# Optimization experiments

Measured on AMD Instinct MI355X. Metric: run time of the kernel, lower is better.

The kernel has to match this reference:

```python
import jax, jax.numpy as jnp
import numpy as np

IN_F = 1024
OUT_F = 4096
BATCH = 1024

def setup_inputs() -> dict:
    key = jax.random.key(0)
    k1, k2, k3, k4 = jax.random.split(key, 4)
    s = np.sqrt(IN_F).astype(np.float32)  # weight init range, as in reset_parameters
    x = jax.random.normal(k1, (BATCH, IN_F), dtype=jnp.float32)
    weights = jax.random.uniform(k2, (OUT_F, IN_F), minval=-s, maxval=s, dtype=jnp.float32)
    centers = 0.1 * jax.random.normal(k3, (OUT_F, IN_F), dtype=jnp.float32)
    # sigmas ~ U(in-0.5, in+0.5); inv_covar = 1/sigmas
    sigmas = jax.random.uniform(k4, (OUT_F, IN_F), minval=IN_F - 0.5, maxval=IN_F + 0.5, dtype=jnp.float32)
    inv_covar = 1.0 / sigmas
    return {"x": x, "weights": weights, "centers": centers, "inv_covar": inv_covar}

def reference(x, weights, centers, inv_covar):
    # linear part with FGN bias: b_i = -sum_j W_ij * C_ij
    biases = -jnp.sum(weights * centers, axis=-1)  # (O,)
    l = x @ weights.T + biases                      # (B, O)
    # diag Mahalanobis: g_bi = sum_j (x_bj - c_ij)^2 * ic_ij^2
    # expanded to GEMMs to avoid the (B, O, I) broadcast intermediate
    ic2 = inv_covar * inv_covar                     # (O, I)
    g = ((x * x) @ ic2.T
         - 2.0 * (x @ (centers * ic2).T)
         + jnp.sum(centers * centers * ic2, axis=-1))  # (B, O)
    return l * jnp.exp(-g)
```

## Files before the change

kernel.cpp:

```cpp
#include <hip/hip_runtime.h>
#include <hip/hip_bf16.h>
#include <stdint.h>


typedef __attribute__((ext_vector_type(8))) __bf16 bf16x8;
typedef __attribute__((ext_vector_type(4))) float f32x4;

__device__ __forceinline__ unsigned short f2bf(float f) {
  union { float f; unsigned int u; } v; v.f = f;
  unsigned int u = v.u;
  unsigned int r = (u + 0x7FFFu + ((u >> 16) & 1u)) >> 16;
  return (unsigned short)r;
}

__global__ __launch_bounds__(256) void prep_rows(
    const float* __restrict__ W, const float* __restrict__ C,
    const float* __restrict__ IC,
    unsigned short* __restrict__ Wb, unsigned short* __restrict__ I2b,
    unsigned short* __restrict__ M2b,
    float* __restrict__ bias, float* __restrict__ dvec) {
  const int wave = threadIdx.x >> 6;
  const int lane = threadIdx.x & 63;
  const int row  = blockIdx.x * 4 + wave;
  const float4* W4 = (const float4*)W + (size_t)row * 256;
  const float4* C4 = (const float4*)C + (size_t)row * 256;
  const float4* I4 = (const float4*)IC + (size_t)row * 256;
  ushort4* Wo = (ushort4*)Wb + (size_t)row * 256;
  ushort4* Io = (ushort4*)I2b + (size_t)row * 256;
  ushort4* Mo = (ushort4*)M2b + (size_t)row * 256;
  float swc = 0.f, sd = 0.f;
#pragma unroll
  for (int p = 0; p < 4; ++p) {
    int idx = lane + p * 64;
    float4 w = W4[idx], c = C4[idx], ic = I4[idx];
    float i2x = ic.x * ic.x, i2y = ic.y * ic.y, i2z = ic.z * ic.z, i2w = ic.w * ic.w;
    swc += w.x * c.x + w.y * c.y + w.z * c.z + w.w * c.w;
    sd  += c.x * c.x * i2x + c.y * c.y * i2y + c.z * c.z * i2z + c.w * c.w * i2w;
    ushort4 a, b, m;
    a.x = f2bf(w.x); a.y = f2bf(w.y); a.z = f2bf(w.z); a.w = f2bf(w.w);
    b.x = f2bf(i2x); b.y = f2bf(i2y); b.z = f2bf(i2z); b.w = f2bf(i2w);
    m.x = f2bf(-2.f * c.x * i2x); m.y = f2bf(-2.f * c.y * i2y);
    m.z = f2bf(-2.f * c.z * i2z); m.w = f2bf(-2.f * c.w * i2w);
    Wo[idx] = a; Io[idx] = b; Mo[idx] = m;
  }
#pragma unroll
  for (int off = 32; off > 0; off >>= 1) {
    swc += __shfl_down(swc, off);
    sd  += __shfl_down(sd, off);
  }
  if (lane == 0) { bias[row] = -swc; dvec[row] = sd; }
}

__global__ __launch_bounds__(256) void prep_x(
    const float* __restrict__ X,
    unsigned short* __restrict__ Xb, unsigned short* __restrict__ Qb) {
  int idx = blockIdx.x * 256 + threadIdx.x;
  float4 x = ((const float4*)X)[idx];
  ushort4 a, b;
  a.x = f2bf(x.x); a.y = f2bf(x.y); a.z = f2bf(x.z); a.w = f2bf(x.w);
  b.x = f2bf(x.x * x.x); b.y = f2bf(x.y * x.y);
  b.z = f2bf(x.z * x.z); b.w = f2bf(x.w * x.w);
  ((ushort4*)Xb)[idx] = a;
  ((ushort4*)Qb)[idx] = b;
}

#define GLD16(gp, lp)                                                          \
  __builtin_amdgcn_global_load_lds(                                            \
      (const __attribute__((address_space(1))) unsigned int*)(gp),             \
      (__attribute__((address_space(3))) unsigned int*)(lp), 16, 0, 0)

__global__ __launch_bounds__(256) void fgn_gemm(
    const unsigned short* __restrict__ Xb, const unsigned short* __restrict__ Qb,
    const unsigned short* __restrict__ Wb, const unsigned short* __restrict__ I2b,
    const unsigned short* __restrict__ M2b,
    const float* __restrict__ bias, const float* __restrict__ dvec,
    float* __restrict__ out) {
  __shared__ unsigned short sx[64 * 32];
  __shared__ unsigned short sq[64 * 32];
  __shared__ unsigned short sw[128 * 32];
  __shared__ unsigned short si[128 * 32];
  __shared__ unsigned short sm[128 * 32];
  const int t = threadIdx.x;
  const int m0 = blockIdx.y * 64;
  const int n0 = blockIdx.x * 128;

  const int arow = t >> 2;
  const int acol = (t & 3) * 8;
  const unsigned short* gx  = Xb  + (size_t)(m0 + arow) * 1024 + acol;
  const unsigned short* gq  = Qb  + (size_t)(m0 + arow) * 1024 + acol;
  const unsigned short* gw0 = Wb  + (size_t)(n0 + arow) * 1024 + acol;
  const unsigned short* gw1 = Wb  + (size_t)(n0 + 64 + arow) * 1024 + acol;
  const unsigned short* gi0 = I2b + (size_t)(n0 + arow) * 1024 + acol;
  const unsigned short* gi1 = I2b + (size_t)(n0 + 64 + arow) * 1024 + acol;
  const unsigned short* gm0 = M2b + (size_t)(n0 + arow) * 1024 + acol;
  const unsigned short* gm1 = M2b + (size_t)(n0 + 64 + arow) * 1024 + acol;

  const int wave = t >> 6, lane = t & 63;
  const int wm = (wave & 1) * 32;
  const int wn = (wave >> 1) * 64;
  const int fm = lane & 15;
  const int q  = lane >> 4;

  f32x4 accL[2][4], accG[2][4];
#pragma unroll
  for (int mt = 0; mt < 2; ++mt)
#pragma unroll
    for (int nt = 0; nt < 4; ++nt) { accL[mt][nt] = (f32x4)0.f; accG[mt][nt] = (f32x4)0.f; }

  for (int k0 = 0; k0 < 1024; k0 += 32) {
    __syncthreads();
    GLD16(gx,  &sx[t * 8]);
    GLD16(gq,  &sq[t * 8]);
    GLD16(gw0, &sw[t * 8]);
    GLD16(gw1, &sw[2048 + t * 8]);
    GLD16(gi0, &si[t * 8]);
    GLD16(gi1, &si[2048 + t * 8]);
    GLD16(gm0, &sm[t * 8]);
    GLD16(gm1, &sm[2048 + t * 8]);
    gx += 32; gq += 32; gw0 += 32; gw1 += 32;
    gi0 += 32; gi1 += 32; gm0 += 32; gm1 += 32;
    __syncthreads();

    bf16x8 ax[2], aq[2], bw[4], bi[4], bm[4];
#pragma unroll
    for (int mt = 0; mt < 2; ++mt) {
      int r = wm + mt * 16 + fm;
      ax[mt] = *(const bf16x8*)&sx[r * 32 + q * 8];
      aq[mt] = *(const bf16x8*)&sq[r * 32 + q * 8];
    }
#pragma unroll
    for (int nt = 0; nt < 4; ++nt) {
      int r = wn + nt * 16 + fm;
      bw[nt] = *(const bf16x8*)&sw[r * 32 + q * 8];
      bi[nt] = *(const bf16x8*)&si[r * 32 + q * 8];
      bm[nt] = *(const bf16x8*)&sm[r * 32 + q * 8];
    }
#pragma unroll
    for (int mt = 0; mt < 2; ++mt)
#pragma unroll
      for (int nt = 0; nt < 4; ++nt) {
        accL[mt][nt] = __builtin_amdgcn_mfma_f32_16x16x32_bf16(ax[mt], bw[nt], accL[mt][nt], 0, 0, 0);
        accG[mt][nt] = __builtin_amdgcn_mfma_f32_16x16x32_bf16(aq[mt], bi[nt], accG[mt][nt], 0, 0, 0);
        accG[mt][nt] = __builtin_amdgcn_mfma_f32_16x16x32_bf16(ax[mt], bm[nt], accG[mt][nt], 0, 0, 0);
      }
  }

#pragma unroll
  for (int nt = 0; nt < 4; ++nt) {
    int gcol = n0 + wn + nt * 16 + fm;
    float bn = bias[gcol], dn = dvec[gcol];
#pragma unroll
    for (int mt = 0; mt < 2; ++mt) {
      int growb = m0 + wm + mt * 16 + q * 4;
#pragma unroll
      for (int r = 0; r < 4; ++r) {
        float l = accL[mt][nt][r] + bn;
        float g = accG[mt][nt][r] + dn;
        out[(size_t)(growb + r) * 4096 + gcol] = l * __expf(-g);
      }
    }
  }
}

extern "C" void kernel_launch(void* const* d_in, const int* in_sizes, int n_in,
                              void* d_out, int out_size, void* d_ws, size_t ws_size,
                              hipStream_t stream) {
  const float* x  = (const float*)d_in[0];
  const float* W  = (const float*)d_in[1];
  const float* C  = (const float*)d_in[2];
  const float* IC = (const float*)d_in[3];
  float* out = (float*)d_out;

  char* ws = (char*)d_ws;
  unsigned short* Wb  = (unsigned short*)(ws);
  unsigned short* I2b = (unsigned short*)(ws + (8u << 20));
  unsigned short* M2b = (unsigned short*)(ws + (16u << 20));
  unsigned short* Xb  = (unsigned short*)(ws + (24u << 20));
  unsigned short* Qb  = (unsigned short*)(ws + (26u << 20));
  float* bias = (float*)(ws + (28u << 20));
  float* dvec = (float*)(ws + (28u << 20) + 16384);

  hipLaunchKernelGGL(prep_rows, dim3(1024), dim3(256), 0, stream, W, C, IC,
                     Wb, I2b, M2b, bias, dvec);
  hipLaunchKernelGGL(prep_x, dim3(1024), dim3(256), 0, stream, x, Xb, Qb);
  hipLaunchKernelGGL(fgn_gemm, dim3(32, 16), dim3(256), 0, stream,
                     Xb, Qb, Wb, I2b, M2b, bias, dvec, out);
}
```

Measured before the change: 139.1 us.

## Enlarge GEMM tile, double-buffer LDS, swizzle, use 32x32 MFMA, merge prep kernels

Merges the two prep kernels into one launch. The GEMM tile grows from 64x128 to 128x128, switches to 32x32x16 MFMA instructions, and double-buffers LDS so the next K-slice is loaded while the current one is computed. LDS columns are XOR-swizzled to cut bank conflicts. The larger tile halves the grid to 256 blocks at one block per CU, which lowers occupancy and may under-fill the 256 CUs while improving data reuse.

```diff
diff --git a/kernel.cpp b/kernel.cpp
--- a/kernel.cpp
+++ b/kernel.cpp
@@ -4,7 +4,7 @@
 
 
 typedef __attribute__((ext_vector_type(8))) __bf16 bf16x8;
-typedef __attribute__((ext_vector_type(4))) float f32x4;
+typedef __attribute__((ext_vector_type(16))) float f32x16;
 
 __device__ __forceinline__ unsigned short f2bf(float f) {
   union { float f; unsigned int u; } v; v.f = f;
@@ -13,55 +13,59 @@
   return (unsigned short)r;
 }
 
-__global__ __launch_bounds__(256) void prep_rows(
-    const float* __restrict__ W, const float* __restrict__ C,
-    const float* __restrict__ IC,
+__global__ __launch_bounds__(256) void prep(
+    const float* __restrict__ X, const float* __restrict__ W,
+    const float* __restrict__ C, const float* __restrict__ IC,
     unsigned short* __restrict__ Wb, unsigned short* __restrict__ I2b,
     unsigned short* __restrict__ M2b,
+    unsigned short* __restrict__ Xb, unsigned short* __restrict__ Qb,
     float* __restrict__ bias, float* __restrict__ dvec) {
-  const int wave = threadIdx.x >> 6;
-  const int lane = threadIdx.x & 63;
-  const int row  = blockIdx.x * 4 + wave;
-  const float4* W4 = (const float4*)W + (size_t)row * 256;
-  const float4* C4 = (const float4*)C + (size_t)row * 256;
-  const float4* I4 = (const float4*)IC + (size_t)row * 256;
-  ushort4* Wo = (ushort4*)Wb + (size_t)row * 256;
-  ushort4* Io = (ushort4*)I2b + (size_t)row * 256;
-  ushort4* Mo = (ushort4*)M2b + (size_t)row * 256;
-  float swc = 0.f, sd = 0.f;
-#pragma unroll
-  for (int p = 0; p < 4; ++p) {
-    int idx = lane + p * 64;
-    float4 w = W4[idx], c = C4[idx], ic = I4[idx];
-    float i2x = ic.x * ic.x, i2y = ic.y * ic.y, i2z = ic.z * ic.z, i2w = ic.w * ic.w;
-    swc += w.x * c.x + w.y * c.y + w.z * c.z + w.w * c.w;
-    sd  += c.x * c.x * i2x + c.y * c.y * i2y + c.z * c.z * i2z + c.w * c.w * i2w;
-    ushort4 a, b, m;
-    a.x = f2bf(w.x); a.y = f2bf(w.y); a.z = f2bf(w.z); a.w = f2bf(w.w);
-    b.x = f2bf(i2x); b.y = f2bf(i2y); b.z = f2bf(i2z); b.w = f2bf(i2w);
-    m.x = f2bf(-2.f * c.x * i2x); m.y = f2bf(-2.f * c.y * i2y);
-    m.z = f2bf(-2.f * c.z * i2z); m.w = f2bf(-2.f * c.w * i2w);
-    Wo[idx] = a; Io[idx] = b; Mo[idx] = m;
-  }
-#pragma unroll
-  for (int off = 32; off > 0; off >>= 1) {
-    swc += __shfl_down(swc, off);
-    sd  += __shfl_down(sd, off);
-  }
-  if (lane == 0) { bias[row] = -swc; dvec[row] = sd; }
-}
-
-__global__ __launch_bounds__(256) void prep_x(
-    const float* __restrict__ X,
-    unsigned short* __restrict__ Xb, unsigned short* __restrict__ Qb) {
-  int idx = blockIdx.x * 256 + threadIdx.x;
-  float4 x = ((const float4*)X)[idx];
-  ushort4 a, b;
-  a.x = f2bf(x.x); a.y = f2bf(x.y); a.z = f2bf(x.z); a.w = f2bf(x.w);
-  b.x = f2bf(x.x * x.x); b.y = f2bf(x.y * x.y);
-  b.z = f2bf(x.z * x.z); b.w = f2bf(x.w * x.w);
-  ((ushort4*)Xb)[idx] = a;
-  ((ushort4*)Qb)[idx] = b;
+  const int b = blockIdx.x;
+  if (b < 1024) {
+    const int wave = threadIdx.x >> 6;
+    const int lane = threadIdx.x & 63;
+    const int row  = b * 4 + wave;
+    const float4* W4 = (const float4*)W + (size_t)row * 256;
+    const float4* C4 = (const float4*)C + (size_t)row * 256;
+    const float4* I4 = (const float4*)IC + (size_t)row * 256;
+    ushort4* Wo = (ushort4*)Wb + (size_t)row * 256;
+    ushort4* Io = (ushort4*)I2b + (size_t)row * 256;
+    ushort4* Mo = (ushort4*)M2b + (size_t)row * 256;
+    float swc = 0.f, sd = 0.f;
+#pragma unroll
+    for (int p = 0; p < 4; ++p) {
+      int idx = lane + p * 64;
+      float4 w = W4[idx], c = C4[idx], ic = I4[idx];
+      float i2x = ic.x * ic.x, i2y = ic.y * ic.y, i2z = ic.z * ic.z, i2w = ic.w * ic.w;
+      swc += w.x * c.x + w.y * c.y + w.z * c.z + w.w * c.w;
+      sd  += c.x * c.x * i2x + c.y * c.y * i2y + c.z * c.z * i2z + c.w * c.w * i2w;
+      ushort4 a, bb, m;
+      a.x = f2bf(w.x); a.y = f2bf(w.y); a.z = f2bf(w.z); a.w = f2bf(w.w);
+      bb.x = f2bf(i2x); bb.y = f2bf(i2y); bb.z = f2bf(i2z); bb.w = f2bf(i2w);
+      m.x = f2bf(-2.f * c.x * i2x); m.y = f2bf(-2.f * c.y * i2y);
+      m.z = f2bf(-2.f * c.z * i2z); m.w = f2bf(-2.f * c.w * i2w);
+      Wo[idx] = a; Io[idx] = bb; Mo[idx] = m;
+    }
+#pragma unroll
+    for (int off = 32; off > 0; off >>= 1) {
+      swc += __shfl_down(swc, off);
+      sd  += __shfl_down(sd, off);
+    }
+    if (lane == 0) { bias[row] = -swc; dvec[row] = sd; }
+  } else {
+    const int xb = b - 1024;
+#pragma unroll
+    for (int j = 0; j < 4; ++j) {
+      int idx = xb * 1024 + j * 256 + threadIdx.x;
+      float4 v = ((const float4*)X)[idx];
+      ushort4 a, q;
+      a.x = f2bf(v.x); a.y = f2bf(v.y); a.z = f2bf(v.z); a.w = f2bf(v.w);
+      q.x = f2bf(v.x * v.x); q.y = f2bf(v.y * v.y);
+      q.z = f2bf(v.z * v.z); q.w = f2bf(v.w * v.w);
+      ((ushort4*)Xb)[idx] = a;
+      ((ushort4*)Qb)[idx] = q;
+    }
+  }
 }
 
 #define GLD16(gp, lp)                                                          \
@@ -69,97 +73,117 @@
       (const __attribute__((address_space(1))) unsigned int*)(gp),             \
       (__attribute__((address_space(3))) unsigned int*)(lp), 16, 0, 0)
 
-__global__ __launch_bounds__(256) void fgn_gemm(
+__global__ __launch_bounds__(256, 1) void fgn_gemm(
     const unsigned short* __restrict__ Xb, const unsigned short* __restrict__ Qb,
     const unsigned short* __restrict__ Wb, const unsigned short* __restrict__ I2b,
     const unsigned short* __restrict__ M2b,
     const float* __restrict__ bias, const float* __restrict__ dvec,
     float* __restrict__ out) {
-  __shared__ unsigned short sx[64 * 32];
-  __shared__ unsigned short sq[64 * 32];
-  __shared__ unsigned short sw[128 * 32];
-  __shared__ unsigned short si[128 * 32];
-  __shared__ unsigned short sm[128 * 32];
+  __shared__ unsigned short lds[2][5][4096];
   const int t = threadIdx.x;
-  const int m0 = blockIdx.y * 64;
+  const int m0 = blockIdx.y * 128;
   const int n0 = blockIdx.x * 128;
 
-  const int arow = t >> 2;
-  const int acol = (t & 3) * 8;
-  const unsigned short* gx  = Xb  + (size_t)(m0 + arow) * 1024 + acol;
-  const unsigned short* gq  = Qb  + (size_t)(m0 + arow) * 1024 + acol;
-  const unsigned short* gw0 = Wb  + (size_t)(n0 + arow) * 1024 + acol;
-  const unsigned short* gw1 = Wb  + (size_t)(n0 + 64 + arow) * 1024 + acol;
-  const unsigned short* gi0 = I2b + (size_t)(n0 + arow) * 1024 + acol;
-  const unsigned short* gi1 = I2b + (size_t)(n0 + 64 + arow) * 1024 + acol;
-  const unsigned short* gm0 = M2b + (size_t)(n0 + arow) * 1024 + acol;
-  const unsigned short* gm1 = M2b + (size_t)(n0 + 64 + arow) * 1024 + acol;
+  const int srow = t >> 2;
+  const int gco  = ((t & 3) ^ ((t >> 3) & 3)) * 8;
+
+  const unsigned short* g0 = Xb  + (size_t)(m0 + srow) * 1024 + gco;
+  const unsigned short* g1 = Qb  + (size_t)(m0 + srow) * 1024 + gco;
+  const unsigned short* g2 = Wb  + (size_t)(n0 + srow) * 1024 + gco;
+  const unsigned short* g3 = I2b + (size_t)(n0 + srow) * 1024 + gco;
+  const unsigned short* g4 = M2b + (size_t)(n0 + srow) * 1024 + gco;
+
+#define STAGE(B, S)                                                            \
+  do {                                                                         \
+    const int ko = (S) * 32;                                                   \
+    GLD16(g0 + ko,         &lds[B][0][t * 8]);                                 \
+    GLD16(g0 + ko + 65536, &lds[B][0][2048 + t * 8]);                          \
+    GLD16(g1 + ko,         &lds[B][1][t * 8]);                                 \
+    GLD16(g1 + ko + 65536, &lds[B][1][2048 + t * 8]);                          \
+    GLD16(g2 + ko,         &lds[B][2][t * 8]);                                 \
+    GLD16(g2 + ko + 65536, &lds[B][2][2048 + t * 8]);                          \
+    GLD16(g3 + ko,         &lds[B][3][t * 8]);                                 \
+    GLD16(g3 + ko + 65536, &lds[B][3][2048 + t * 8]);                          \
+    GLD16(g4 + ko,         &lds[B][4][t * 8]);                                 \
+    GLD16(g4 + ko + 65536, &lds[B][4][2048 + t * 8]);                          \
+  } while (0)
 
   const int wave = t >> 6, lane = t & 63;
-  const int wm = (wave & 1) * 32;
-  const int wn = (wave >> 1) * 64;
-  const int fm = lane & 15;
-  const int q  = lane >> 4;
-
-  f32x4 accL[2][4], accG[2][4];
-#pragma unroll
-  for (int mt = 0; mt < 2; ++mt)
-#pragma unroll
-    for (int nt = 0; nt < 4; ++nt) { accL[mt][nt] = (f32x4)0.f; accG[mt][nt] = (f32x4)0.f; }
-
-  for (int k0 = 0; k0 < 1024; k0 += 32) {
+  const int wx = wave & 1, wy = wave >> 1;
+  const int ln = lane & 31, kh = lane >> 5;
+  const int sw = (ln >> 1) & 3;
+
+  int aoff[2], boff[2];
+#pragma unroll
+  for (int i = 0; i < 2; ++i) {
+    aoff[i] = (wy * 64 + i * 32 + ln) * 32;
+    boff[i] = (wx * 64 + i * 32 + ln) * 32;
+  }
+
+  f32x16 accL[2][2], accG[2][2];
+#pragma unroll
+  for (int i = 0; i < 2; ++i)
+#pragma unroll
+    for (int j = 0; j < 2; ++j) { accL[i][j] = (f32x16)0.f; accG[i][j] = (f32x16)0.f; }
+
+#define COMPUTE(B)                                                             \
+  do {                                                                         \
+    _Pragma("unroll")                                                          \
+    for (int ks = 0; ks < 2; ++ks) {                                           \
+      const int co = ((ks * 2 + kh) ^ sw) * 8;                                 \
+      bf16x8 ax[2], aq[2], bw[2], bi[2], bm[2];                                \
+      _Pragma("unroll")                                                        \
+      for (int i = 0; i < 2; ++i) {                                            \
+        ax[i] = *(const bf16x8*)&lds[B][0][aoff[i] + co];                      \
+        aq[i] = *(const bf16x8*)&lds[B][1][aoff[i] + co];                      \
+        bw[i] = *(const bf16x8*)&lds[B][2][boff[i] + co];                      \
+        bi[i] = *(const bf16x8*)&lds[B][3][boff[i] + co];                      \
+        bm[i] = *(const bf16x8*)&lds[B][4][boff[i] + co];                      \
+      }                                                                        \
+      _Pragma("unroll")                                                        \
+      for (int mt = 0; mt < 2; ++mt)                                           \
+        _Pragma("unroll")                                                      \
+        for (int nt = 0; nt < 2; ++nt) {                                       \
+          accL[mt][nt] = __builtin_amdgcn_mfma_f32_32x32x16_bf16(              \
+              ax[mt], bw[nt], accL[mt][nt], 0, 0, 0);                          \
+          accG[mt][nt] = __builtin_amdgcn_mfma_f32_32x32x16_bf16(              \
+              aq[mt], bi[nt], accG[mt][nt], 0, 0, 0);                          \
+          accG[mt][nt] = __builtin_amdgcn_mfma_f32_32x32x16_bf16(              \
+              ax[mt], bm[nt], accG[mt][nt], 0, 0, 0);                          \
+        }                                                                      \
+    }                                                                          \
+  } while (0)
+
+  STAGE(0, 0);
+  __syncthreads();
+#pragma unroll 1
+  for (int p = 0; p < 16; ++p) {
+    STAGE(1, 2 * p + 1);
+    COMPUTE(0);
     __syncthreads();
-    GLD16(gx,  &sx[t * 8]);
-    GLD16(gq,  &sq[t * 8]);
-    GLD16(gw0, &sw[t * 8]);
-    GLD16(gw1, &sw[2048 + t * 8]);
-    GLD16(gi0, &si[t * 8]);
-    GLD16(gi1, &si[2048 + t * 8]);
-    GLD16(gm0, &sm[t * 8]);
-    GLD16(gm1, &sm[2048 + t * 8]);
-    gx += 32; gq += 32; gw0 += 32; gw1 += 32;
-    gi0 += 32; gi1 += 32; gm0 += 32; gm1 += 32;
+    if (p < 15) STAGE(0, 2 * p + 2);
+    COMPUTE(1);
     __syncthreads();
-
-    bf16x8 ax[2], aq[2], bw[4], bi[4], bm[4];
+  }
+
+#pragma unroll
+  for (int nt = 0; nt < 2; ++nt) {
+    int col = n0 + wx * 64 + nt * 32 + ln;
+    float bn = bias[col], dn = dvec[col];
 #pragma unroll
     for (int mt = 0; mt < 2; ++mt) {
-      int r = wm + mt * 16 + fm;
-      ax[mt] = *(const bf16x8*)&sx[r * 32 + q * 8];
-      aq[mt] = *(const bf16x8*)&sq[r * 32 + q * 8];
-    }
-#pragma unroll
-    for (int nt = 0; nt < 4; ++nt) {
-      int r = wn + nt * 16 + fm;
-      bw[nt] = *(const bf16x8*)&sw[r * 32 + q * 8];
-      bi[nt] = *(const bf16x8*)&si[r * 32 + q * 8];
-      bm[nt] = *(const bf16x8*)&sm[r * 32 + q * 8];
-    }
-#pragma unroll
-    for (int mt = 0; mt < 2; ++mt)
-#pragma unroll
-      for (int nt = 0; nt < 4; ++nt) {
-        accL[mt][nt] = __builtin_amdgcn_mfma_f32_16x16x32_bf16(ax[mt], bw[nt], accL[mt][nt], 0, 0, 0);
-        accG[mt][nt] = __builtin_amdgcn_mfma_f32_16x16x32_bf16(aq[mt], bi[nt], accG[mt][nt], 0, 0, 0);
-        accG[mt][nt] = __builtin_amdgcn_mfma_f32_16x16x32_bf16(ax[mt], bm[nt], accG[mt][nt], 0, 0, 0);
+      int rb = m0 + wy * 64 + mt * 32 + 4 * kh;
+#pragma unroll
+      for (int r = 0; r < 16; ++r) {
+        int row = rb + (r & 3) + 8 * (r >> 2);
+        float l  = accL[mt][nt][r] + bn;
+        float gg = accG[mt][nt][r] + dn;
+        out[(size_t)row * 4096 + col] = l * __expf(-gg);
       }
-  }
-
-#pragma unroll
-  for (int nt = 0; nt < 4; ++nt) {
-    int gcol = n0 + wn + nt * 16 + fm;
-    float bn = bias[gcol], dn = dvec[gcol];
-#pragma unroll
-    for (int mt = 0; mt < 2; ++mt) {
-      int growb = m0 + wm + mt * 16 + q * 4;
-#pragma unroll
-      for (int r = 0; r < 4; ++r) {
-        float l = accL[mt][nt][r] + bn;
-        float g = accG[mt][nt][r] + dn;
-        out[(size_t)(growb + r) * 4096 + gcol] = l * __expf(-g);
-      }
-    }
-  }
+    }
+  }
+#undef STAGE
+#undef COMPUTE
 }
 
 extern "C" void kernel_launch(void* const* d_in, const int* in_sizes, int n_in,
@@ -180,9 +204,8 @@
   float* bias = (float*)(ws + (28u << 20));
   float* dvec = (float*)(ws + (28u << 20) + 16384);
 
-  hipLaunchKernelGGL(prep_rows, dim3(1024), dim3(256), 0, stream, W, C, IC,
-                     Wb, I2b, M2b, bias, dvec);
-  hipLaunchKernelGGL(prep_x, dim3(1024), dim3(256), 0, stream, x, Xb, Qb);
-  hipLaunchKernelGGL(fgn_gemm, dim3(32, 16), dim3(256), 0, stream,
+  hipLaunchKernelGGL(prep, dim3(1280), dim3(256), 0, stream, x, W, C, IC,
+                     Wb, I2b, M2b, Xb, Qb, bias, dvec);
+  hipLaunchKernelGGL(fgn_gemm, dim3(32, 8), dim3(256), 0, stream,
                      Xb, Qb, Wb, I2b, M2b, bias, dvec, out);
 }
```

Result: no change. 138.3 us (-0.6%).
